# Kernel optimization log

Measured on AMD Instinct MI355X. Metric: run time of the kernel, lower is better.

Reference implementation:

```python
import math
import jax, jax.numpy as jnp
import numpy as np

B, L, C, H = 4, 2048, 1024, 16
D = C // H  # head dim = 64

def setup_inputs() -> dict:
    key = jax.random.key(0)
    k1, k2, k3 = jax.random.split(key, 3)
    x = jax.random.normal(k1, (B, L, C), dtype=jnp.float32)
    w_attn = jax.random.normal(k2, (C, 3 * C), dtype=jnp.float32) * (1.0 / math.sqrt(C))
    w_proj = jax.random.normal(k3, (C, C), dtype=jnp.float32) * (1.0 / math.sqrt(C))
    return {"x": x, "w_attn": w_attn, "w_proj": w_proj}

def reference(x, w_attn, w_proj):
    b, l, c = x.shape
    s = x @ w_attn                      # (B,L,3C)
    q, k, v = s[:, :, :c], s[:, :, c:2 * c], s[:, :, 2 * c:]
    # (B,L,H,D) -> (B,H,L,D)
    q = q.reshape(b, l, H, D).transpose(0, 2, 1, 3)
    k = k.reshape(b, l, H, D).transpose(0, 2, 1, 3)
    v = v.reshape(b, l, H, D).transpose(0, 2, 1, 3)
    att = jnp.einsum('bhqd,bhkd->bhqk', q, k) * (1.0 / math.sqrt(D))
    causal = jnp.tril(jnp.ones((l, l), dtype=bool))
    att = jnp.where(causal[None, None], att, -jnp.inf)
    att = jax.nn.softmax(att, axis=-1)
    y = jnp.einsum('bhqk,bhkd->bhqd', att, v)
    y = y.transpose(0, 2, 1, 3).reshape(b, l, c)
    return y @ w_proj
```

## Files before the change

### kernel.cpp

```cpp
#include <hip/hip_runtime.h>
#include <math.h>

typedef unsigned short u16;
typedef unsigned int u32;
typedef __bf16 bf16x8 __attribute__((ext_vector_type(8)));
typedef float f32x4 __attribute__((ext_vector_type(4)));
typedef float f32x16 __attribute__((ext_vector_type(16)));
typedef u16 u16x4 __attribute__((ext_vector_type(4)));
typedef u16 u16x8 __attribute__((ext_vector_type(8)));
typedef u32 u32x4 __attribute__((ext_vector_type(4)));

#define MFMA16(a, b, c) __builtin_amdgcn_mfma_f32_16x16x32_bf16((a), (b), (c), 0, 0, 0)
#define MFMA32(a, b, c) __builtin_amdgcn_mfma_f32_32x32x16_bf16((a), (b), (c), 0, 0, 0)

#define GLL16(g, l)                                                   \
  __builtin_amdgcn_global_load_lds(                                   \
      (const __attribute__((address_space(1))) void*)(g),             \
      (__attribute__((address_space(3))) void*)(l), 16, 0, 0)

__device__ __forceinline__ u16 f2bf(float f) {
  __bf16 h = (__bf16)f;
  return __builtin_bit_cast(u16, h);
}
__device__ __forceinline__ u32 pack2(float a, float b) {
  return (u32)f2bf(a) | ((u32)f2bf(b) << 16);
}
__device__ __forceinline__ float exp2a(float x) {
  float r;
  asm("v_exp_f32 %0, %1" : "=v"(r) : "v"(x));
  return r;
}

__global__ __launch_bounds__(256) void cvt_f32_bf16(const float* __restrict__ in,
                                                    u16* __restrict__ out) {
  size_t i = ((size_t)blockIdx.x * 256 + threadIdx.x) * 4;
  float4 v = *(const float4*)(in + i);
  u16x4 o;
  o[0] = f2bf(v.x); o[1] = f2bf(v.y); o[2] = f2bf(v.z); o[3] = f2bf(v.w);
  *(u16x4*)(out + i) = o;
}

__global__ __launch_bounds__(256) void transpose_w(const float* __restrict__ in,
                                                   u16* __restrict__ out,
                                                   int R, int Cn) {
  __shared__ u16 tile[64][72];
  const int t = threadIdx.x;
  const int tr = blockIdx.y * 64;
  const int tc = blockIdx.x * 64;
#pragma unroll
  for (int p = 0; p < 4; ++p) {
    int chunk = p * 256 + t;
    int r = chunk >> 4, cq = chunk & 15;
    float4 v = *(const float4*)(in + (size_t)(tr + r) * Cn + tc + cq * 4);
    tile[r][cq * 4 + 0] = f2bf(v.x);
    tile[r][cq * 4 + 1] = f2bf(v.y);
    tile[r][cq * 4 + 2] = f2bf(v.z);
    tile[r][cq * 4 + 3] = f2bf(v.w);
  }
  __syncthreads();
#pragma unroll
  for (int p = 0; p < 2; ++p) {
    int chunk = p * 256 + t;
    int c = chunk >> 3, rg = chunk & 7;
    u16x8 v;
#pragma unroll
    for (int i = 0; i < 8; ++i) v[i] = tile[rg * 8 + i][c];
    *(u16x8*)(out + (size_t)(tc + c) * R + tr + rg * 8) = v;
  }
}

__global__ __launch_bounds__(256) void transpose_v(const u16* __restrict__ S,
                                                   u16* __restrict__ VT) {
  __shared__ u16 tile[64][72];
  const int t = threadIdx.x;
  const int lt = blockIdx.x;
  const int bh = blockIdx.y;
  const int b = bh >> 4, h = bh & 15;
  const u16* src = S + ((size_t)b * 2048 + (size_t)lt * 64) * 3072 + 2048 + h * 64;
  u16* dst = VT + (size_t)bh * 64 * 2048 + (size_t)lt * 64;
#pragma unroll
  for (int p = 0; p < 2; ++p) {
    int chunk = p * 256 + t;
    int r = chunk >> 3, cg = chunk & 7;
    u16x8 v = *(const u16x8*)(src + (size_t)r * 3072 + cg * 8);
    *(u16x8*)(&tile[r][cg * 8]) = v;
  }
  __syncthreads();
#pragma unroll
  for (int p = 0; p < 2; ++p) {
    int chunk = p * 256 + t;
    int d = chunk >> 3, rg = chunk & 7;
    u16x8 v;
#pragma unroll
    for (int i = 0; i < 8; ++i) v[i] = tile[rg * 8 + i][d];
    *(u16x8*)(dst + (size_t)d * 2048 + rg * 8) = v;
  }
}

template <bool OUTF32>
__global__ __launch_bounds__(256, 2) void gemm_bt(const u16* __restrict__ A,
                                                  const u16* __restrict__ BT,
                                                  void* __restrict__ Cp,
                                                  int M, int N, int K) {
  __shared__ u16 As[128 * 64];
  __shared__ u16 Bs[128 * 64];
  const int tid = threadIdx.x;
  const int lane = tid & 63;
  const int wid = tid >> 6;
  const int wr = wid >> 1, wc = wid & 1;
  const int rl = lane & 15, kg = lane >> 4;

  const int id = blockIdx.x + gridDim.x * blockIdx.y;
  const int cpx = (gridDim.x * gridDim.y) >> 3;
  const int swz = (id & 7) * cpx + (id >> 3);
  const int bx = swz % gridDim.x;
  const int by = swz / gridDim.x;
  const size_t rowA0 = (size_t)by * 128;
  const size_t rowB0 = (size_t)bx * 128;

  const int r_st = tid >> 3;
  const int cg_st = tid & 7;

  f32x4 acc[4][4] = {};

  for (int kb = 0; kb < K; kb += 64) {
    __syncthreads();
#pragma unroll
    for (int it = 0; it < 4; ++it) {
      int r = it * 32 + r_st;
      int cgs = cg_st ^ (r & 7);
      GLL16(A + (rowA0 + r) * K + kb + cgs * 8, As + (size_t)r * 64 + cg_st * 8);
      GLL16(BT + (rowB0 + r) * K + kb + cgs * 8, Bs + (size_t)r * 64 + cg_st * 8);
    }
    __syncthreads();

    bf16x8 af[2][4], bfr[2][4];
#pragma unroll
    for (int kk = 0; kk < 2; ++kk) {
      int c8 = kk * 4 + kg;
#pragma unroll
      for (int m = 0; m < 4; ++m) {
        int ra = wr * 64 + m * 16 + rl;
        af[kk][m] = *(const bf16x8*)(As + (size_t)ra * 64 + (size_t)((c8 ^ (ra & 7)) * 8));
        int rb = wc * 64 + m * 16 + rl;
        bfr[kk][m] = *(const bf16x8*)(Bs + (size_t)rb * 64 + (size_t)((c8 ^ (rb & 7)) * 8));
      }
    }
#pragma unroll
    for (int kk = 0; kk < 2; ++kk)
#pragma unroll
      for (int m = 0; m < 4; ++m)
#pragma unroll
        for (int n = 0; n < 4; ++n)
          acc[m][n] = MFMA16(af[kk][m], bfr[kk][n], acc[m][n]);
  }

#pragma unroll
  for (int m = 0; m < 4; ++m)
#pragma unroll
    for (int n = 0; n < 4; ++n)
#pragma unroll
      for (int j = 0; j < 4; ++j) {
        size_t r = rowA0 + wr * 64 + m * 16 + kg * 4 + j;
        size_t c = rowB0 + wc * 64 + n * 16 + rl;
        if constexpr (OUTF32)
          ((float*)Cp)[r * N + c] = acc[m][n][j];
        else
          ((u16*)Cp)[r * N + c] = f2bf(acc[m][n][j]);
      }
}

__global__ __launch_bounds__(256) void attn(const u16* __restrict__ S,
                                            const u16* __restrict__ VT,
                                            u16* __restrict__ Y) {
  __shared__ u16 Ks[2][64 * 64];
  __shared__ u16 Vs[2][64 * 64];
  const int bh = blockIdx.x;
  const int g = blockIdx.y;
  const int t1 = 31 - g;
  const int b = bh >> 4, h = bh & 15;
  const int tid = threadIdx.x, lane = tid & 63, wid = tid >> 6;
  const int ql = lane & 31;
  const int hi = lane >> 5;
  const int grp = wid >> 1;
  const int hw = wid & 1;
  const int myt = grp ? t1 : g;
  const int qrow = myt * 64 + hw * 32 + ql;

  const u16* Sq = S + (size_t)b * 2048 * 3072 + h * 64;
  const u16* Sk = Sq + 1024;
  const u16* Vh = VT + (size_t)bh * 64 * 2048;

  const int sr = tid >> 3, scg = tid & 7;

#define STAGE(buf, kt)                                                          \
  {                                                                             \
    _Pragma("unroll") for (int it = 0; it < 2; ++it) {                          \
      int r = it * 32 + sr;                                                     \
      int cs = scg ^ (r & 7);               \
      GLL16(Sk + (size_t)((kt) * 64 + r) * 3072 + cs * 8,                       \
            &Ks[buf][r * 64 + scg * 8]);                                        \
      GLL16(Vh + (size_t)r * 2048 + (kt) * 64 + cs * 8,                         \
            &Vs[buf][r * 64 + scg * 8]);                                        \
    }                                                                           \
  }

  const float SC = 0.125f * 1.44269504088896f;
  bf16x8 qf[4];
#pragma unroll
  for (int s4 = 0; s4 < 4; ++s4) {
    bf16x8 q = *(const bf16x8*)(Sq + (size_t)qrow * 3072 + s4 * 16 + hi * 8);
    bf16x8 qs;
#pragma unroll
    for (int i = 0; i < 8; ++i) qs[i] = (__bf16)((float)q[i] * SC);
    qf[s4] = qs;
  }

  f32x16 O0 = {}, O1 = {};
  float mj = -INFINITY, lj = 0.f;

  STAGE(0, 0);
  __syncthreads();

  for (int kt = 0; kt <= t1; ++kt) {
    const int cur = kt & 1;
    if (kt < t1) STAGE(cur ^ 1, kt + 1);
    const u16* Ksb = Ks[cur];
    const u16* Vsb = Vs[cur];

    const bool active = (grp == 1) || (kt <= g);
    if (active) {
      f32x16 s0 = {}, s1 = {};
      __builtin_amdgcn_s_setprio(1);
#pragma unroll
      for (int s4 = 0; s4 < 4; ++s4) {
        int cix = (2 * s4 + hi) ^ (ql & 7);
        bf16x8 kf0 = *(const bf16x8*)(Ksb + (size_t)ql * 64 + cix * 8);
        bf16x8 kf1 = *(const bf16x8*)(Ksb + (size_t)(32 + ql) * 64 + cix * 8);
        s0 = MFMA32(kf0, qf[s4], s0);
        s1 = MFMA32(kf1, qf[s4], s1);
      }
      __builtin_amdgcn_s_setprio(0);

      if (kt == myt) {
        const int lim = hw * 32 + ql;
#pragma unroll
        for (int r = 0; r < 16; ++r) {
          int c0 = (r & 3) + 8 * (r >> 2) + 4 * hi;
          s0[r] = (c0 <= lim) ? s0[r] : -INFINITY;
          s1[r] = (32 + c0 <= lim) ? s1[r] : -INFINITY;
        }
      }

      float t16[16];
#pragma unroll
      for (int r = 0; r < 16; ++r) t16[r] = fmaxf(s0[r], s1[r]);
#pragma unroll
      for (int off = 8; off >= 1; off >>= 1)
#pragma unroll
        for (int i = 0; i < 8; ++i)
          if (i < off) t16[i] = fmaxf(t16[i], t16[i + off]);
      float rmax = fmaxf(t16[0], __shfl_xor(t16[0], 32));

      if (__any(rmax > mj + 8.0f)) {
        float mn = (rmax > mj + 8.0f) ? rmax : mj;
        float scl = exp2a(mj - mn);
        mj = mn;
        lj *= scl;
#pragma unroll
        for (int r = 0; r < 16; ++r) { O0[r] *= scl; O1[r] *= scl; }
      }

#pragma unroll
      for (int r = 0; r < 16; ++r) {
        s0[r] = exp2a(s0[r] - mj);
        s1[r] = exp2a(s1[r] - mj);
      }
      float a16[16];
#pragma unroll
      for (int r = 0; r < 16; ++r) a16[r] = s0[r] + s1[r];
#pragma unroll
      for (int off = 8; off >= 1; off >>= 1)
#pragma unroll
        for (int i = 0; i < 8; ++i)
          if (i < off) a16[i] += a16[i + off];
      lj += a16[0] + __shfl_xor(a16[0], 32);

      __builtin_amdgcn_s_setprio(1);
#pragma unroll
      for (int Sstep = 0; Sstep < 4; ++Sstep) {
        const int kb = Sstep >> 1, s = Sstep & 1;
        float e0 = kb ? s1[8 * s + 0] : s0[8 * s + 0];
        float e1 = kb ? s1[8 * s + 1] : s0[8 * s + 1];
        float e2 = kb ? s1[8 * s + 2] : s0[8 * s + 2];
        float e3 = kb ? s1[8 * s + 3] : s0[8 * s + 3];
        float f0 = kb ? s1[8 * s + 4] : s0[8 * s + 4];
        float f1 = kb ? s1[8 * s + 5] : s0[8 * s + 5];
        float f2 = kb ? s1[8 * s + 6] : s0[8 * s + 6];
        float f3 = kb ? s1[8 * s + 7] : s0[8 * s + 7];
        u32 a0 = pack2(e0, e1), a1 = pack2(e2, e3);
        u32 b0 = pack2(f0, f1), b1 = pack2(f2, f3);
        u32 s0w = hi ? a0 : b0;
        u32 s1w = hi ? a1 : b1;
        u32 r0 = (u32)__shfl_xor((int)s0w, 32);
        u32 r1 = (u32)__shfl_xor((int)s1w, 32);
        u32x4 pw;
        pw[0] = hi ? r0 : a0;
        pw[1] = hi ? r1 : a1;
        pw[2] = hi ? b0 : r0;
        pw[3] = hi ? b1 : r1;
        bf16x8 pf = __builtin_bit_cast(bf16x8, pw);
        int cix = (2 * Sstep + hi) ^ (ql & 7);
        bf16x8 vf0 = *(const bf16x8*)(Vsb + (size_t)ql * 64 + cix * 8);
        bf16x8 vf1 = *(const bf16x8*)(Vsb + (size_t)(32 + ql) * 64 + cix * 8);
        O0 = MFMA32(vf0, pf, O0);
        O1 = MFMA32(vf1, pf, O1);
      }
      __builtin_amdgcn_s_setprio(0);
    }
    __syncthreads();
  }

  const float inv = 1.0f / lj;
  u16* yrow = Y + (size_t)(b * 2048 + qrow) * 1024 + h * 64;
#pragma unroll
  for (int db = 0; db < 2; ++db)
#pragma unroll
    for (int rq = 0; rq < 4; ++rq) {
      u16x4 o;
#pragma unroll
      for (int j = 0; j < 4; ++j) {
        float v = (db ? O1[rq * 4 + j] : O0[rq * 4 + j]) * inv;
        o[j] = f2bf(v);
      }
      *(u16x4*)(yrow + db * 32 + 8 * rq + 4 * hi) = o;
    }
#undef STAGE
}

extern "C" void kernel_launch(void* const* d_in, const int* in_sizes, int n_in,
                              void* d_out, int out_size, void* d_ws, size_t ws_size,
                              hipStream_t stream) {
  const float* x = (const float*)d_in[0];
  const float* w_attn = (const float*)d_in[1];
  const float* w_proj = (const float*)d_in[2];
  float* out = (float*)d_out;

  u16* S = (u16*)d_ws;
  u16* WT1 = S + (size_t)8192 * 3072;
  u16* WT2 = WT1 + (size_t)3072 * 1024;
  u16* VT = WT2 + (size_t)1024 * 1024;
  u16* Y = VT + (size_t)64 * 64 * 2048;
  u16* XB = Y + (size_t)8192 * 1024;

  cvt_f32_bf16<<<8192, 256, 0, stream>>>(x, XB);
  transpose_w<<<dim3(3072 / 64, 1024 / 64), 256, 0, stream>>>(w_attn, WT1, 1024, 3072);
  transpose_w<<<dim3(1024 / 64, 1024 / 64), 256, 0, stream>>>(w_proj, WT2, 1024, 1024);
  gemm_bt<false><<<dim3(3072 / 128, 8192 / 128), 256, 0, stream>>>(XB, WT1, S, 8192, 3072, 1024);
  transpose_v<<<dim3(32, 64), 256, 0, stream>>>(S, VT);
  attn<<<dim3(64, 16), 256, 0, stream>>>(S, VT, Y);
  gemm_bt<true><<<dim3(1024 / 128, 8192 / 128), 256, 0, stream>>>(Y, WT2, out, 8192, 1024, 1024);
}
```

Baseline: 286.9 us.

## Rewrite GEMM as 256x256 tile with triple-buffered LDS pipeline

Replaces the 128x128, 256-thread GEMM with a 256x256 tile, 512-thread kernel. It uses a BK=32 K-step with three LDS buffers, prefetching two stages ahead via global_load_lds, and splits each step into two MFMA halves interleaved with staging loads. It also raises MFMA priority with setprio and uses fine-grained vmcnt waits instead of full syncthreads. The aim is higher data reuse per tile and hiding global load latency behind compute. The trade-offs are more registers and fewer blocks: the projection GEMM now launches only 128 blocks, which may underfill the GPU.

Measured after the change: 296.6 us. 3.4% more time.

```diff
diff --git a/kernel.cpp b/kernel.cpp
--- a/kernel.cpp
+++ b/kernel.cpp
@@ -98,16 +98,17 @@
 }
 
 template <bool OUTF32>
-__global__ __launch_bounds__(256, 2) void gemm_bt(const u16* __restrict__ A,
+__global__ __launch_bounds__(512, 2) void gemm256(const u16* __restrict__ A,
                                                   const u16* __restrict__ BT,
                                                   void* __restrict__ Cp,
                                                   int M, int N, int K) {
-  __shared__ u16 As[128 * 64];
-  __shared__ u16 Bs[128 * 64];
+  __shared__ u16 As[3][256 * 32];
+  __shared__ u16 Bs[3][256 * 32];
   const int tid = threadIdx.x;
   const int lane = tid & 63;
   const int wid = tid >> 6;
-  const int wr = wid >> 1, wc = wid & 1;
+  const int wm = wid >> 2;
+  const int wn = wid & 3;
   const int rl = lane & 15, kg = lane >> 4;
 
   const int id = blockIdx.x + gridDim.x * blockIdx.y;
@@ -115,58 +116,101 @@
   const int swz = (id & 7) * cpx + (id >> 3);
   const int bx = swz % gridDim.x;
   const int by = swz / gridDim.x;
-  const size_t rowA0 = (size_t)by * 128;
-  const size_t rowB0 = (size_t)bx * 128;
-
-  const int r_st = tid >> 3;
-  const int cg_st = tid & 7;
-
-  f32x4 acc[4][4] = {};
-
-  for (int kb = 0; kb < K; kb += 64) {
-    __syncthreads();
-#pragma unroll
-    for (int it = 0; it < 4; ++it) {
-      int r = it * 32 + r_st;
-      int cgs = cg_st ^ (r & 7);
-      GLL16(A + (rowA0 + r) * K + kb + cgs * 8, As + (size_t)r * 64 + cg_st * 8);
-      GLL16(BT + (rowB0 + r) * K + kb + cgs * 8, Bs + (size_t)r * 64 + cg_st * 8);
+  const size_t rowA0 = (size_t)by * 256;
+  const size_t rowB0 = (size_t)bx * 256;
+
+  const int r_st = tid >> 2;
+  const int cg_st = tid & 3;
+
+  const int KT = K >> 5;
+
+  f32x4 acc[8][4] = {};
+
+#define STG_A(buf, kt)                                                      \
+  { _Pragma("unroll") for (int half = 0; half < 2; ++half) {                \
+      int r = half * 128 + r_st;                                            \
+      int cgs = cg_st ^ ((r >> 1) & 3);        \
+      GLL16(A + (rowA0 + r) * K + (kt) * 32 + cgs * 8,                      \
+            &As[buf][r * 32 + cg_st * 8]); } }
+#define STG_B(buf, kt)                                                      \
+  { _Pragma("unroll") for (int half = 0; half < 2; ++half) {                \
+      int r = half * 128 + r_st;                                            \
+      int cgs = cg_st ^ ((r >> 1) & 3);                                     \
+      GLL16(BT + (rowB0 + r) * K + (kt) * 32 + cgs * 8,                     \
+            &Bs[buf][r * 32 + cg_st * 8]); } }
+
+  STG_A(0, 0); STG_B(0, 0);
+  STG_A(1, 1); STG_B(1, 1);
+  asm volatile("s_waitcnt vmcnt(4)" ::: "memory");
+  __builtin_amdgcn_s_barrier();
+
+  int cur = 0;
+#pragma unroll 1
+  for (int kt = 0; kt < KT; ++kt) {
+    const u16* Asb = &As[cur][0];
+    const u16* Bsb = &Bs[cur][0];
+    int nxt = cur + 2; if (nxt >= 3) nxt -= 3;
+    const bool more = (kt < KT - 2);
+
+    bf16x8 bfr[4];
+#pragma unroll
+    for (int n = 0; n < 4; ++n) {
+      int row = wn * 64 + n * 16 + rl;
+      bfr[n] = *(const bf16x8*)(Bsb + (size_t)row * 32 +
+                                (size_t)((kg ^ ((row >> 1) & 3)) * 8));
     }
-    __syncthreads();
-
-    bf16x8 af[2][4], bfr[2][4];
-#pragma unroll
-    for (int kk = 0; kk < 2; ++kk) {
-      int c8 = kk * 4 + kg;
-#pragma unroll
-      for (int m = 0; m < 4; ++m) {
-        int ra = wr * 64 + m * 16 + rl;
-        af[kk][m] = *(const bf16x8*)(As + (size_t)ra * 64 + (size_t)((c8 ^ (ra & 7)) * 8));
-        int rb = wc * 64 + m * 16 + rl;
-        bfr[kk][m] = *(const bf16x8*)(Bs + (size_t)rb * 64 + (size_t)((c8 ^ (rb & 7)) * 8));
-      }
+    bf16x8 af[4];
+#pragma unroll
+    for (int m = 0; m < 4; ++m) {
+      int row = wm * 128 + m * 16 + rl;
+      af[m] = *(const bf16x8*)(Asb + (size_t)row * 32 +
+                               (size_t)((kg ^ ((row >> 1) & 3)) * 8));
     }
-#pragma unroll
-    for (int kk = 0; kk < 2; ++kk)
-#pragma unroll
-      for (int m = 0; m < 4; ++m)
-#pragma unroll
-        for (int n = 0; n < 4; ++n)
-          acc[m][n] = MFMA16(af[kk][m], bfr[kk][n], acc[m][n]);
-  }
-
-#pragma unroll
-  for (int m = 0; m < 4; ++m)
+    if (more) STG_A(nxt, kt + 2);
+    __builtin_amdgcn_s_setprio(1);
+#pragma unroll
+    for (int m = 0; m < 4; ++m)
+#pragma unroll
+      for (int n = 0; n < 4; ++n)
+        acc[m][n] = MFMA16(af[m], bfr[n], acc[m][n]);
+    __builtin_amdgcn_s_setprio(0);
+    __builtin_amdgcn_s_barrier();
+
+#pragma unroll
+    for (int m = 0; m < 4; ++m) {
+      int row = wm * 128 + (4 + m) * 16 + rl;
+      af[m] = *(const bf16x8*)(Asb + (size_t)row * 32 +
+                               (size_t)((kg ^ ((row >> 1) & 3)) * 8));
+    }
+    if (more) STG_B(nxt, kt + 2);
+    __builtin_amdgcn_s_setprio(1);
+#pragma unroll
+    for (int m = 0; m < 4; ++m)
+#pragma unroll
+      for (int n = 0; n < 4; ++n)
+        acc[4 + m][n] = MFMA16(af[m], bfr[n], acc[4 + m][n]);
+    __builtin_amdgcn_s_setprio(0);
+    if (more) asm volatile("s_waitcnt vmcnt(4)" ::: "memory");
+    else      asm volatile("s_waitcnt vmcnt(0)" ::: "memory");
+    __builtin_amdgcn_s_barrier();
+
+    cur += 1; if (cur >= 3) cur -= 3;
+  }
+#undef STG_A
+#undef STG_B
+
+#pragma unroll
+  for (int mi = 0; mi < 8; ++mi)
 #pragma unroll
     for (int n = 0; n < 4; ++n)
 #pragma unroll
       for (int j = 0; j < 4; ++j) {
-        size_t r = rowA0 + wr * 64 + m * 16 + kg * 4 + j;
-        size_t c = rowB0 + wc * 64 + n * 16 + rl;
+        size_t r = rowA0 + wm * 128 + mi * 16 + kg * 4 + j;
+        size_t c = rowB0 + wn * 64 + n * 16 + rl;
         if constexpr (OUTF32)
-          ((float*)Cp)[r * N + c] = acc[m][n][j];
+          ((float*)Cp)[r * N + c] = acc[mi][n][j];
         else
-          ((u16*)Cp)[r * N + c] = f2bf(acc[m][n][j]);
+          ((u16*)Cp)[r * N + c] = f2bf(acc[mi][n][j]);
       }
 }
 
@@ -356,8 +400,8 @@
   cvt_f32_bf16<<<8192, 256, 0, stream>>>(x, XB);
   transpose_w<<<dim3(3072 / 64, 1024 / 64), 256, 0, stream>>>(w_attn, WT1, 1024, 3072);
   transpose_w<<<dim3(1024 / 64, 1024 / 64), 256, 0, stream>>>(w_proj, WT2, 1024, 1024);
-  gemm_bt<false><<<dim3(3072 / 128, 8192 / 128), 256, 0, stream>>>(XB, WT1, S, 8192, 3072, 1024);
+  gemm256<false><<<dim3(3072 / 256, 8192 / 256), 512, 0, stream>>>(XB, WT1, S, 8192, 3072, 1024);
   transpose_v<<<dim3(32, 64), 256, 0, stream>>>(S, VT);
   attn<<<dim3(64, 16), 256, 0, stream>>>(S, VT, Y);
-  gemm_bt<true><<<dim3(1024 / 128, 8192 / 128), 256, 0, stream>>>(Y, WT2, out, 8192, 1024, 1024);
-}
+  gemm256<true><<<dim3(1024 / 256, 8192 / 256), 512, 0, stream>>>(Y, WT2, out, 8192, 1024, 1024);
+}
```
